# Kernel tuning notes

Measured on AMD Instinct MI355X. Metric: run time of the kernel, lower is better.

## Reference

```python
import jax, jax.numpy as jnp
import numpy as np

N = 100000
R = 32
E = 3200000
EMB = 128
H = 32
B = 16
C = 16

def setup_inputs() -> dict:
    key = jax.random.key(0)
    ks = jax.random.split(key, 10)
    def xavier(k, shape):
        fan_in, fan_out = shape[-2], shape[-1]
        gain = jnp.sqrt(2.0)  # relu gain
        std = gain * jnp.sqrt(2.0 / (fan_in + fan_out))
        return jax.random.normal(k, shape, jnp.float32) * std
    return {
        'embeddings': xavier(ks[0], (N, EMB)),
        'comps1': xavier(ks[1], (R, B)),
        'bases1': xavier(ks[2], (B, EMB, H)),
        'comps2': xavier(ks[3], (R, B)),
        'bases2': xavier(ks[4], (B, H, C)),
        'bias1': jnp.zeros((H,), jnp.float32),
        'bias2': jnp.zeros((C,), jnp.float32),
        'rel': jax.random.randint(ks[5], (E,), 0, R, jnp.int32),
        'fr': jax.random.randint(ks[6], (E,), 0, N, jnp.int32),
        'to': jax.random.randint(ks[7], (E,), 0, N, jnp.int32),
    }

def reference(embeddings, comps1, bases1, comps2, bases2, bias1, bias2, rel, fr, to):
    n, emb = embeddings.shape
    r = comps1.shape[0]
    h = bases1.shape[2]
    # edge normalization: vals = 1 / rowsum of vertical adjacency, row = rel*n + fr
    seg = rel * n + fr  # [E]
    deg = jax.ops.segment_sum(jnp.ones_like(fr, jnp.float32), seg, num_segments=r * n)
    vals = 1.0 / deg[seg]  # [E]
    # layer 1: basis-composed weights, per-relation transform, hor-graph spmm
    w1 = jnp.einsum('rb,beh->reh', comps1, bases1)          # [r,emb,h]
    xw = jnp.einsum('ne,reh->rnh', embeddings, w1)           # [r,n,h]
    # hor_graph @ xw.view(r*n,h): hidden1[fr] += vals * xw[rel, to]
    hidden1 = jax.ops.segment_sum(vals[:, None] * xw[rel, to], fr, num_segments=n)  # [n,h]
    hidden1 = jax.nn.relu(hidden1 + bias1)
    # layer 2: ver-graph spmm then relation-combining einsum
    w2 = jnp.einsum('rb,bhc->rhc', comps2, bases2)           # [r,h,c]
    hidden2 = jax.ops.segment_sum(vals[:, None] * hidden1[to], seg, num_segments=r * n)
    hidden2 = hidden2.reshape(r, n, h)
    out = jnp.einsum('rhc,rnh->nc', w2, hidden2)             # [n,c]
    return out + bias2
```

## Files before the change

### kernel.cpp

```cpp
#include <hip/hip_runtime.h>

#define N_NODES 100000
#define N_PAD   100096
#define E_EDGES 3200000
#define NB      392
#define BCAP    12288
#define EPB     2048

typedef float f32x4 __attribute__((ext_vector_type(4)));
typedef __bf16 bf16x8 __attribute__((ext_vector_type(8)));

__device__ __forceinline__ float b2f(unsigned int u) {
    union { unsigned int i; float f; } x; x.i = u << 16; return x.f;
}
__device__ __forceinline__ unsigned short f2b(float f) {
    union { float f; unsigned int i; } x; x.f = f;
    unsigned int u = x.i + 0x7FFFu + ((x.i >> 16) & 1u);
    return (unsigned short)(u >> 16);
}

__global__ __launch_bounds__(256) void kcur(int* __restrict__ gCursor) {
    int id = blockIdx.x * 256 + threadIdx.x;
    if (id < NB) gCursor[id] = id * BCAP;
}

__global__ __launch_bounds__(256) void kemb(const float* __restrict__ emb,
                                            unsigned short* __restrict__ embb) {
    int id = blockIdx.x * 256 + threadIdx.x;
    if (id >= N_PAD * 128 / 8) return;
    size_t base = (size_t)id * 8;
    ushort4 o0 = {0, 0, 0, 0}, o1 = {0, 0, 0, 0};
    if (base < (size_t)N_NODES * 128) {
        float4 v0 = *(const float4*)(emb + base);
        float4 v1 = *(const float4*)(emb + base + 4);
        o0.x = f2b(v0.x); o0.y = f2b(v0.y); o0.z = f2b(v0.z); o0.w = f2b(v0.w);
        o1.x = f2b(v1.x); o1.y = f2b(v1.y); o1.z = f2b(v1.z); o1.w = f2b(v1.w);
    }
    *(ushort4*)(embb + base) = o0;
    *(ushort4*)(embb + base + 4) = o1;
}

__global__ __launch_bounds__(256) void kw1(const float* __restrict__ comps1,
                                           const float* __restrict__ bases1,
                                           unsigned short* __restrict__ w1T) {
    int id = blockIdx.x * 256 + threadIdx.x;
    if (id >= 1024 * 128) return;
    int k = id & 127, j = id >> 7;
    int r = j >> 5, h = j & 31;
    float s = 0.f;
#pragma unroll
    for (int b = 0; b < 16; b++)
        s += comps1[r * 16 + b] * bases1[b * 4096 + k * 32 + h];
    w1T[(size_t)j * 128 + k] = f2b(s);
}

__global__ __launch_bounds__(256) void kw2(const float* __restrict__ comps2,
                                           const float* __restrict__ bases2,
                                           unsigned short* __restrict__ w2T) {
    int id = blockIdx.x * 256 + threadIdx.x;
    if (id >= 512 * 32) return;
    int h = id & 31, j = id >> 5;
    int r = j >> 4, c = j & 15;
    float s = 0.f;
#pragma unroll
    for (int b = 0; b < 16; b++)
        s += comps2[r * 16 + b] * bases2[b * 512 + h * 16 + c];
    w2T[(size_t)j * 32 + h] = f2b(s);
}

__global__ __launch_bounds__(256) void kbinA(const int* __restrict__ rel,
                                             const int* __restrict__ fr,
                                             const int* __restrict__ to,
                                             int* __restrict__ gCursor,
                                             unsigned int* __restrict__ stage) {
    __shared__ int cnt[NB];
    __shared__ int base[NB];
    int tid = threadIdx.x;
    int g0 = blockIdx.x * (EPB / 4);
    for (int i = tid; i < NB; i += 256) cnt[i] = 0;
    __syncthreads();
#pragma unroll
    for (int i = 0; i < EPB / 1024; i++) {
        int g = g0 + i * 256 + tid;
        if (g < E_EDGES / 4) {
            int4 f4 = ((const int4*)fr)[g];
            atomicAdd(&cnt[f4.x >> 8], 1);
            atomicAdd(&cnt[f4.y >> 8], 1);
            atomicAdd(&cnt[f4.z >> 8], 1);
            atomicAdd(&cnt[f4.w >> 8], 1);
        }
    }
    __syncthreads();
    for (int i = tid; i < NB; i += 256) {
        base[i] = atomicAdd(&gCursor[i], cnt[i]);
        cnt[i] = 0;
    }
    __syncthreads();
#pragma unroll
    for (int i = 0; i < EPB / 1024; i++) {
        int g = g0 + i * 256 + tid;
        if (g < E_EDGES / 4) {
            int4 f4 = ((const int4*)fr)[g];
            int4 r4 = ((const int4*)rel)[g];
            int4 t4 = ((const int4*)to)[g];
            int fa[4] = {f4.x, f4.y, f4.z, f4.w};
            int ra[4] = {r4.x, r4.y, r4.z, r4.w};
            int ta[4] = {t4.x, t4.y, t4.z, t4.w};
#pragma unroll
            for (int u = 0; u < 4; u++) {
                int b = fa[u] >> 8;
                int rank = atomicAdd(&cnt[b], 1);
                stage[base[b] + rank] =
                    ((unsigned int)(fa[u] & 255) << 22) | ((unsigned int)ra[u] << 17) | (unsigned int)ta[u];
            }
        }
    }
}

__global__ __launch_bounds__(512) void kscan(const int* __restrict__ gCursor,
                                             int* __restrict__ bucketBase) {
    __shared__ int a[512], b[512];
    int t = threadIdx.x;
    int v = (t < NB) ? (gCursor[t] - t * BCAP) : 0;
    a[t] = v;
    __syncthreads();
    int* src = a; int* dst = b;
    for (int ofs = 1; ofs < 512; ofs <<= 1) {
        int x = src[t];
        if (t >= ofs) x += src[t - ofs];
        __syncthreads();
        dst[t] = x;
        __syncthreads();
        int* tmp = src; src = dst; dst = tmp;
    }
    if (t < NB) bucketBase[t] = src[t] - v;
}

__global__ __launch_bounds__(256) void kscatter2(const unsigned int* __restrict__ stage,
                                                 const int* __restrict__ gCursor,
                                                 const int* __restrict__ bucketBase,
                                                 int* __restrict__ rowptr,
                                                 unsigned int* __restrict__ packed) {
    __shared__ int hist[256], hexcl[256], rk[256], sa[256], sb[256];
    __shared__ int hist2[256 * 32];
    int b = blockIdx.x, t = threadIdx.x;
    int nb = gCursor[b] - b * BCAP;
    int sbase = b * BCAP;
    int gbase = bucketBase[b];
    int nb4 = nb >> 2;
    hist[t] = 0; rk[t] = 0;
    for (int i = t; i < 256 * 32; i += 256) hist2[i] = 0;
    __syncthreads();
    for (int i4 = t; i4 < nb4; i4 += 256) {
        uint4 p4 = ((const uint4*)(stage + sbase))[i4];
        unsigned int pa[4] = {p4.x, p4.y, p4.z, p4.w};
#pragma unroll
        for (int u = 0; u < 4; u++) {
            atomicAdd(&hist[pa[u] >> 22], 1);
            atomicAdd(&hist2[((pa[u] >> 22) << 5) | ((pa[u] >> 17) & 31)], 1);
        }
    }
    for (int i = (nb4 << 2) + t; i < nb; i += 256) {
        unsigned int pk = stage[sbase + i];
        atomicAdd(&hist[pk >> 22], 1);
        atomicAdd(&hist2[((pk >> 22) << 5) | ((pk >> 17) & 31)], 1);
    }
    __syncthreads();
    int v = hist[t];
    sa[t] = v;
    __syncthreads();
    int* src = sa; int* dst = sb;
    for (int ofs = 1; ofs < 256; ofs <<= 1) {
        int x = src[t];
        if (t >= ofs) x += src[t - ofs];
        __syncthreads();
        dst[t] = x;
        __syncthreads();
        int* tmp = src; src = dst; dst = tmp;
    }
    int excl = src[t] - v;
    hexcl[t] = excl;
    rowptr[b * 256 + t] = gbase + excl;
    __syncthreads();
    for (int i4 = t; i4 < nb4; i4 += 256) {
        uint4 p4 = ((const uint4*)(stage + sbase))[i4];
        unsigned int pa[4] = {p4.x, p4.y, p4.z, p4.w};
#pragma unroll
        for (int u = 0; u < 4; u++) {
            int frlo = pa[u] >> 22;
            int rank = atomicAdd(&rk[frlo], 1);
            int dg = min(hist2[(frlo << 5) | ((pa[u] >> 17) & 31)], 1023);
            packed[gbase + hexcl[frlo] + rank] = ((unsigned int)dg << 22) | (pa[u] & 0x3FFFFFu);
        }
    }
    for (int i = (nb4 << 2) + t; i < nb; i += 256) {
        unsigned int pk = stage[sbase + i];
        int frlo = pk >> 22;
        int rank = atomicAdd(&rk[frlo], 1);
        int dg = min(hist2[(frlo << 5) | ((pk >> 17) & 31)], 1023);
        packed[gbase + hexcl[frlo] + rank] = ((unsigned int)dg << 22) | (pk & 0x3FFFFFu);
    }
}

__global__ __launch_bounds__(256) void gemm1(const unsigned short* __restrict__ embb,
                                             const unsigned short* __restrict__ w1T,
                                             unsigned short* __restrict__ xw) {
    __shared__ unsigned short ldsT[4 * 16 * 136];
    int id = blockIdx.x;
    int xcd = id & 7, w = id >> 3;
    int bn = w & 15, mgl = w >> 4;
    int mg = mgl * 8 + xcd;
    if (mg >= 98) return;
    int lane = threadIdx.x & 63, wave = threadIdx.x >> 6;
    int m_ = lane & 15, q = lane >> 4;
    unsigned short* tw = &ldsT[wave * 16 * 136];
    bf16x8 B[4][4];
    const unsigned short* Bbase = w1T + (size_t)(bn * 64 + m_) * 128 + q * 8;
#pragma unroll
    for (int j = 0; j < 4; j++)
#pragma unroll
        for (int k0 = 0; k0 < 4; k0++)
            B[j][k0] = *(const bf16x8*)(Bbase + j * 16 * 128 + k0 * 32);
    int mrow0 = mg * 1024 + wave * 16;
    const unsigned short* Abase = embb + (size_t)(mrow0 + m_) * 128 + q * 8;
    bf16x8 a0[4], a1[4];
    if (mrow0 < N_PAD) {
#pragma unroll
        for (int k0 = 0; k0 < 4; k0++)
            a0[k0] = *(const bf16x8*)(Abase + k0 * 32);
    }
#pragma unroll
    for (int t = 0; t < 16; t++) {
        int m0 = mrow0 + t * 64;
        if (m0 >= N_PAD) break;
        bf16x8* acur = (t & 1) ? a1 : a0;
        bf16x8* anext = (t & 1) ? a0 : a1;
        if (t < 15 && m0 + 64 < N_PAD) {
#pragma unroll
            for (int k0 = 0; k0 < 4; k0++)
                anext[k0] = *(const bf16x8*)(Abase + (size_t)(t + 1) * 64 * 128 + k0 * 32);
        }
        f32x4 acc[4] = {};
#pragma unroll
        for (int k0 = 0; k0 < 4; k0++)
#pragma unroll
            for (int j = 0; j < 4; j++)
                acc[j] = __builtin_amdgcn_mfma_f32_16x16x32_bf16(B[j][k0], acur[k0], acc[j], 0, 0, 0);
#pragma unroll
        for (int jj = 0; jj < 4; jj++) {
            ushort4 s;
            s.x = f2b(acc[jj][0]); s.y = f2b(acc[jj][1]);
            s.z = f2b(acc[jj][2]); s.w = f2b(acc[jj][3]);
            *(ushort4*)(tw + m_ * 136 + jj * 16 + q * 4) = s;
        }
        __asm__ volatile("s_waitcnt lgkmcnt(0)" ::: "memory");
#pragma unroll
        for (int ri = 0; ri < 2; ri++) {
            int row = (lane >> 3) + ri * 8;
            int c = lane & 7;
            uint4 v = *(const uint4*)(tw + row * 136 + c * 8);
            int grow = m0 + row;
            if (grow < N_NODES)
                *(uint4*)(xw + (size_t)grow * 1024 + bn * 64 + c * 8) = v;
        }
        __asm__ volatile("s_waitcnt lgkmcnt(0)" ::: "memory");
    }
}

__global__ __launch_bounds__(256) void edge1csr(const unsigned int* __restrict__ packed,
                                                const int* __restrict__ rowptr,
                                                const unsigned short* __restrict__ xw,
                                                const float* __restrict__ bias1,
                                                unsigned short* __restrict__ h1b) {
    __shared__ unsigned int ebuf[4 * 64];
    __shared__ float vbuf[4 * 64];
    int wave = threadIdx.x >> 6, lane = threadIdx.x & 63;
    int f = blockIdx.x * 4 + wave;
    if (f >= N_NODES) return;
    int s = rowptr[f], k = rowptr[f + 1] - s;
    int sub = lane & 7, p = lane >> 3;
    f32x4 acc = {0.f, 0.f, 0.f, 0.f};
    for (int base = 0; base < k; base += 64) {
        int e = base + lane;
        if (e < k) {
            unsigned int pk = packed[s + e];
            ebuf[wave * 64 + lane] = pk;
            vbuf[wave * 64 + lane] = 1.0f / (float)(pk >> 22);
        }
        int cnum = min(64, k - base);
        int nst = (cnum + 7) >> 3;
#pragma unroll 4
        for (int i = 0; i < nst; i++) {
            int ei = (i << 3) + p;
            if (ei < cnum) {
                unsigned int pk = ebuf[wave * 64 + ei];
                float v = vbuf[wave * 64 + ei];
                int t_ = pk & 0x1FFFF, r = (pk >> 17) & 31;
                ushort4 raw = *(const ushort4*)(xw + (size_t)t_ * 1024 + (r << 5) + (sub << 2));
                acc.x += v * b2f(raw.x); acc.y += v * b2f(raw.y);
                acc.z += v * b2f(raw.z); acc.w += v * b2f(raw.w);
            }
        }
    }
#pragma unroll
    for (int ofs = 8; ofs < 64; ofs <<= 1) {
        acc.x += __shfl_xor(acc.x, ofs, 64);
        acc.y += __shfl_xor(acc.y, ofs, 64);
        acc.z += __shfl_xor(acc.z, ofs, 64);
        acc.w += __shfl_xor(acc.w, ofs, 64);
    }
    if (p == 0) {
        int h = sub << 2;
        ushort4 o;
        o.x = f2b(fmaxf(acc.x + bias1[h + 0], 0.f));
        o.y = f2b(fmaxf(acc.y + bias1[h + 1], 0.f));
        o.z = f2b(fmaxf(acc.z + bias1[h + 2], 0.f));
        o.w = f2b(fmaxf(acc.w + bias1[h + 3], 0.f));
        *(ushort4*)(h1b + (size_t)f * 32 + h) = o;
    }
}

__global__ __launch_bounds__(256) void gemm2(const unsigned short* __restrict__ h1b,
                                             const unsigned short* __restrict__ w2T,
                                             unsigned short* __restrict__ z) {
    __shared__ unsigned short ldsT[4 * 16 * 136];
    int id = blockIdx.x;
    int xcd = id & 7, w = id >> 3;
    int bn = w & 7, mgl = w >> 3;
    int mg = mgl * 8 + xcd;
    if (mg >= 98) return;
    int lane = threadIdx.x & 63, wave = threadIdx.x >> 6;
    int m_ = lane & 15, q = lane >> 4;
    unsigned short* tw = &ldsT[wave * 16 * 136];
    bf16x8 B[4];
    const unsigned short* Bbase = w2T + (size_t)(bn * 64 + m_) * 32 + q * 8;
#pragma unroll
    for (int j = 0; j < 4; j++)
        B[j] = *(const bf16x8*)(Bbase + j * 16 * 32);
    int mrow0 = mg * 1024 + wave * 32;
    const unsigned short* Abase = h1b + (size_t)(mrow0 + m_) * 32 + q * 8;
    bf16x8 a0[2], a1[2];
    if (mrow0 < N_PAD) {
        a0[0] = *(const bf16x8*)(Abase);
        a0[1] = *(const bf16x8*)(Abase + 16 * 32);
    }
#pragma unroll
    for (int t = 0; t < 8; t++) {
        int m0 = mrow0 + t * 128;
        if (m0 >= N_PAD) break;
        bf16x8* acur = (t & 1) ? a1 : a0;
        bf16x8* anext = (t & 1) ? a0 : a1;
        if (t < 7 && m0 + 128 < N_PAD) {
            anext[0] = *(const bf16x8*)(Abase + (size_t)(t + 1) * 128 * 32);
            anext[1] = *(const bf16x8*)(Abase + (size_t)(t + 1) * 128 * 32 + 16 * 32);
        }
        f32x4 acc[2][4] = {};
#pragma unroll
        for (int i = 0; i < 2; i++)
#pragma unroll
            for (int j = 0; j < 4; j++)
                acc[i][j] = __builtin_amdgcn_mfma_f32_16x16x32_bf16(B[j], acur[i], acc[i][j], 0, 0, 0);
#pragma unroll
        for (int i = 0; i < 2; i++) {
#pragma unroll
            for (int jj = 0; jj < 4; jj++) {
                ushort4 s;
                s.x = f2b(acc[i][jj][0]); s.y = f2b(acc[i][jj][1]);
                s.z = f2b(acc[i][jj][2]); s.w = f2b(acc[i][jj][3]);
                *(ushort4*)(tw + m_ * 136 + jj * 16 + q * 4) = s;
            }
            __asm__ volatile("s_waitcnt lgkmcnt(0)" ::: "memory");
#pragma unroll
            for (int ri = 0; ri < 2; ri++) {
                int row = (lane >> 3) + ri * 8;
                int c = lane & 7;
                uint4 v = *(const uint4*)(tw + row * 136 + c * 8);
                int grow = m0 + i * 16 + row;
                if (grow < N_NODES)
                    *(uint4*)(z + (size_t)grow * 512 + bn * 64 + c * 8) = v;
            }
            __asm__ volatile("s_waitcnt lgkmcnt(0)" ::: "memory");
        }
    }
}

__global__ __launch_bounds__(256) void edge2csr(const unsigned int* __restrict__ packed,
                                                const int* __restrict__ rowptr,
                                                const unsigned short* __restrict__ z,
                                                const float* __restrict__ bias2,
                                                float* __restrict__ out) {
    __shared__ unsigned int ebuf[4 * 64];
    __shared__ float vbuf[4 * 64];
    int wave = threadIdx.x >> 6, lane = threadIdx.x & 63;
    int f = blockIdx.x * 4 + wave;
    if (f >= N_NODES) return;
    int s = rowptr[f], k = rowptr[f + 1] - s;
    int sub = lane & 3, p = lane >> 2;
    f32x4 acc = {0.f, 0.f, 0.f, 0.f};
    for (int base = 0; base < k; base += 64) {
        int e = base + lane;
        if (e < k) {
            unsigned int pk = packed[s + e];
            ebuf[wave * 64 + lane] = pk;
            vbuf[wave * 64 + lane] = 1.0f / (float)(pk >> 22);
        }
        int cnum = min(64, k - base);
        int nst = (cnum + 15) >> 4;
#pragma unroll 4
        for (int i = 0; i < nst; i++) {
            int ei = (i << 4) + p;
            if (ei < cnum) {
                unsigned int pk = ebuf[wave * 64 + ei];
                float v = vbuf[wave * 64 + ei];
                int t_ = pk & 0x1FFFF, r = (pk >> 17) & 31;
                ushort4 raw = *(const ushort4*)(z + (size_t)t_ * 512 + (r << 4) + (sub << 2));
                acc.x += v * b2f(raw.x); acc.y += v * b2f(raw.y);
                acc.z += v * b2f(raw.z); acc.w += v * b2f(raw.w);
            }
        }
    }
#pragma unroll
    for (int ofs = 4; ofs < 64; ofs <<= 1) {
        acc.x += __shfl_xor(acc.x, ofs, 64);
        acc.y += __shfl_xor(acc.y, ofs, 64);
        acc.z += __shfl_xor(acc.z, ofs, 64);
        acc.w += __shfl_xor(acc.w, ofs, 64);
    }
    if (p == 0) {
        int c = sub << 2;
        float4 o;
        o.x = acc.x + bias2[c + 0];
        o.y = acc.y + bias2[c + 1];
        o.z = acc.z + bias2[c + 2];
        o.w = acc.w + bias2[c + 3];
        *(float4*)(out + (size_t)f * 16 + c) = o;
    }
}

extern "C" void kernel_launch(void* const* d_in, const int* in_sizes, int n_in,
                              void* d_out, int out_size, void* d_ws, size_t ws_size,
                              hipStream_t stream) {
    (void)in_sizes; (void)n_in; (void)out_size; (void)ws_size;
    const float* emb    = (const float*)d_in[0];
    const float* comps1 = (const float*)d_in[1];
    const float* bases1 = (const float*)d_in[2];
    const float* comps2 = (const float*)d_in[3];
    const float* bases2 = (const float*)d_in[4];
    const float* bias1  = (const float*)d_in[5];
    const float* bias2  = (const float*)d_in[6];
    const int* rel = (const int*)d_in[7];
    const int* fr  = (const int*)d_in[8];
    const int* to  = (const int*)d_in[9];
    float* out = (float*)d_out;
    char* ws = (char*)d_ws;

    int* gCursor         = (int*)(ws);
    int* bucketBase      = (int*)(ws + 2048);
    int* rowptr          = (int*)(ws + 4096);
    unsigned int* packed = (unsigned int*)(ws + 406528);
    unsigned short* h1b  = (unsigned short*)(ws + 13206528);
    unsigned short* w1T  = (unsigned short*)(ws + 19612672);
    unsigned short* w2T  = (unsigned short*)(ws + 19874816);
    unsigned short* embb = (unsigned short*)(ws + 19907584);
    unsigned short* xw   = (unsigned short*)(ws + 45532160);
    unsigned short* z    = xw;
    unsigned int* stage  = (unsigned int*)xw;

    kcur<<<2, 256, 0, stream>>>(gCursor);
    kemb<<<6256, 256, 0, stream>>>(emb, embb);
    kw1<<<512, 256, 0, stream>>>(comps1, bases1, w1T);
    kw2<<<64, 256, 0, stream>>>(comps2, bases2, w2T);
    kbinA<<<(E_EDGES + EPB - 1) / EPB, 256, 0, stream>>>(rel, fr, to, gCursor, stage);
    kscan<<<1, 512, 0, stream>>>(gCursor, bucketBase);
    kscatter2<<<NB, 256, 0, stream>>>(stage, gCursor, bucketBase, rowptr, packed);
    gemm1<<<1664, 256, 0, stream>>>(embb, w1T, xw);
    edge1csr<<<25000, 256, 0, stream>>>(packed, rowptr, xw, bias1, h1b);
    gemm2<<<832, 256, 0, stream>>>(h1b, w2T, z);
    edge2csr<<<25000, 256, 0, stream>>>(packed, rowptr, z, bias2, out);
}
```

Before: 462.7 us.

## Replace CSR build with bucketed edge lists and LDS-atomic aggregation

Result: slower. 1.360 ms (+193.9%).

```diff
diff --git a/kernel.cpp b/kernel.cpp
--- a/kernel.cpp
+++ b/kernel.cpp
@@ -3,8 +3,8 @@
 #define N_NODES 100000
 #define N_PAD   100096
 #define E_EDGES 3200000
-#define NB      392
-#define BCAP    12288
+#define NB      784
+#define BCAP    4864
 #define EPB     2048
 
 typedef float f32x4 __attribute__((ext_vector_type(4)));
@@ -15,29 +15,12 @@
 }
 __device__ __forceinline__ unsigned short f2b(float f) {
     union { float f; unsigned int i; } x; x.f = f;
-    unsigned int u = x.i + 0x7FFFu + ((x.i >> 16) & 1u);
-    return (unsigned short)(u >> 16);
+    return (unsigned short)((x.i + 0x8000u) >> 16);
 }
 
 __global__ __launch_bounds__(256) void kcur(int* __restrict__ gCursor) {
     int id = blockIdx.x * 256 + threadIdx.x;
     if (id < NB) gCursor[id] = id * BCAP;
-}
-
-__global__ __launch_bounds__(256) void kemb(const float* __restrict__ emb,
-                                            unsigned short* __restrict__ embb) {
-    int id = blockIdx.x * 256 + threadIdx.x;
-    if (id >= N_PAD * 128 / 8) return;
-    size_t base = (size_t)id * 8;
-    ushort4 o0 = {0, 0, 0, 0}, o1 = {0, 0, 0, 0};
-    if (base < (size_t)N_NODES * 128) {
-        float4 v0 = *(const float4*)(emb + base);
-        float4 v1 = *(const float4*)(emb + base + 4);
-        o0.x = f2b(v0.x); o0.y = f2b(v0.y); o0.z = f2b(v0.z); o0.w = f2b(v0.w);
-        o1.x = f2b(v1.x); o1.y = f2b(v1.y); o1.z = f2b(v1.z); o1.w = f2b(v1.w);
-    }
-    *(ushort4*)(embb + base) = o0;
-    *(ushort4*)(embb + base + 4) = o1;
 }
 
 __global__ __launch_bounds__(256) void kw1(const float* __restrict__ comps1,
@@ -79,27 +62,12 @@
     int g0 = blockIdx.x * (EPB / 4);
     for (int i = tid; i < NB; i += 256) cnt[i] = 0;
     __syncthreads();
-#pragma unroll
-    for (int i = 0; i < EPB / 1024; i++) {
+    unsigned int wd[8]; int bk[8], rk[8]; bool vld[2];
+#pragma unroll
+    for (int i = 0; i < 2; i++) {
         int g = g0 + i * 256 + tid;
-        if (g < E_EDGES / 4) {
-            int4 f4 = ((const int4*)fr)[g];
-            atomicAdd(&cnt[f4.x >> 8], 1);
-            atomicAdd(&cnt[f4.y >> 8], 1);
-            atomicAdd(&cnt[f4.z >> 8], 1);
-            atomicAdd(&cnt[f4.w >> 8], 1);
-        }
-    }
-    __syncthreads();
-    for (int i = tid; i < NB; i += 256) {
-        base[i] = atomicAdd(&gCursor[i], cnt[i]);
-        cnt[i] = 0;
-    }
-    __syncthreads();
-#pragma unroll
-    for (int i = 0; i < EPB / 1024; i++) {
-        int g = g0 + i * 256 + tid;
-        if (g < E_EDGES / 4) {
+        vld[i] = (g < E_EDGES / 4);
+        if (vld[i]) {
             int4 f4 = ((const int4*)fr)[g];
             int4 r4 = ((const int4*)rel)[g];
             int4 t4 = ((const int4*)to)[g];
@@ -108,101 +76,31 @@
             int ta[4] = {t4.x, t4.y, t4.z, t4.w};
 #pragma unroll
             for (int u = 0; u < 4; u++) {
-                int b = fa[u] >> 8;
-                int rank = atomicAdd(&cnt[b], 1);
-                stage[base[b] + rank] =
-                    ((unsigned int)(fa[u] & 255) << 22) | ((unsigned int)ra[u] << 17) | (unsigned int)ta[u];
-            }
-        }
-    }
-}
-
-__global__ __launch_bounds__(512) void kscan(const int* __restrict__ gCursor,
-                                             int* __restrict__ bucketBase) {
-    __shared__ int a[512], b[512];
-    int t = threadIdx.x;
-    int v = (t < NB) ? (gCursor[t] - t * BCAP) : 0;
-    a[t] = v;
-    __syncthreads();
-    int* src = a; int* dst = b;
-    for (int ofs = 1; ofs < 512; ofs <<= 1) {
-        int x = src[t];
-        if (t >= ofs) x += src[t - ofs];
-        __syncthreads();
-        dst[t] = x;
-        __syncthreads();
-        int* tmp = src; src = dst; dst = tmp;
-    }
-    if (t < NB) bucketBase[t] = src[t] - v;
-}
-
-__global__ __launch_bounds__(256) void kscatter2(const unsigned int* __restrict__ stage,
-                                                 const int* __restrict__ gCursor,
-                                                 const int* __restrict__ bucketBase,
-                                                 int* __restrict__ rowptr,
-                                                 unsigned int* __restrict__ packed) {
-    __shared__ int hist[256], hexcl[256], rk[256], sa[256], sb[256];
-    __shared__ int hist2[256 * 32];
-    int b = blockIdx.x, t = threadIdx.x;
-    int nb = gCursor[b] - b * BCAP;
-    int sbase = b * BCAP;
-    int gbase = bucketBase[b];
-    int nb4 = nb >> 2;
-    hist[t] = 0; rk[t] = 0;
-    for (int i = t; i < 256 * 32; i += 256) hist2[i] = 0;
-    __syncthreads();
-    for (int i4 = t; i4 < nb4; i4 += 256) {
-        uint4 p4 = ((const uint4*)(stage + sbase))[i4];
-        unsigned int pa[4] = {p4.x, p4.y, p4.z, p4.w};
-#pragma unroll
-        for (int u = 0; u < 4; u++) {
-            atomicAdd(&hist[pa[u] >> 22], 1);
-            atomicAdd(&hist2[((pa[u] >> 22) << 5) | ((pa[u] >> 17) & 31)], 1);
-        }
-    }
-    for (int i = (nb4 << 2) + t; i < nb; i += 256) {
-        unsigned int pk = stage[sbase + i];
-        atomicAdd(&hist[pk >> 22], 1);
-        atomicAdd(&hist2[((pk >> 22) << 5) | ((pk >> 17) & 31)], 1);
-    }
-    __syncthreads();
-    int v = hist[t];
-    sa[t] = v;
-    __syncthreads();
-    int* src = sa; int* dst = sb;
-    for (int ofs = 1; ofs < 256; ofs <<= 1) {
-        int x = src[t];
-        if (t >= ofs) x += src[t - ofs];
-        __syncthreads();
-        dst[t] = x;
-        __syncthreads();
-        int* tmp = src; src = dst; dst = tmp;
-    }
-    int excl = src[t] - v;
-    hexcl[t] = excl;
-    rowptr[b * 256 + t] = gbase + excl;
-    __syncthreads();
-    for (int i4 = t; i4 < nb4; i4 += 256) {
-        uint4 p4 = ((const uint4*)(stage + sbase))[i4];
-        unsigned int pa[4] = {p4.x, p4.y, p4.z, p4.w};
-#pragma unroll
-        for (int u = 0; u < 4; u++) {
-            int frlo = pa[u] >> 22;
-            int rank = atomicAdd(&rk[frlo], 1);
-            int dg = min(hist2[(frlo << 5) | ((pa[u] >> 17) & 31)], 1023);
-            packed[gbase + hexcl[frlo] + rank] = ((unsigned int)dg << 22) | (pa[u] & 0x3FFFFFu);
-        }
-    }
-    for (int i = (nb4 << 2) + t; i < nb; i += 256) {
-        unsigned int pk = stage[sbase + i];
-        int frlo = pk >> 22;
-        int rank = atomicAdd(&rk[frlo], 1);
-        int dg = min(hist2[(frlo << 5) | ((pk >> 17) & 31)], 1023);
-        packed[gbase + hexcl[frlo] + rank] = ((unsigned int)dg << 22) | (pk & 0x3FFFFFu);
-    }
-}
-
-__global__ __launch_bounds__(256) void gemm1(const unsigned short* __restrict__ embb,
+                int ix = i * 4 + u;
+                bk[ix] = fa[u] >> 7;
+                wd[ix] = ((unsigned int)(fa[u] & 127) << 22) |
+                         ((unsigned int)ra[u] << 17) | (unsigned int)ta[u];
+                rk[ix] = atomicAdd(&cnt[bk[ix]], 1);
+            }
+        }
+    }
+    __syncthreads();
+    for (int i = tid; i < NB; i += 256)
+        base[i] = atomicAdd(&gCursor[i], cnt[i]);
+    __syncthreads();
+#pragma unroll
+    for (int i = 0; i < 2; i++) {
+        if (vld[i]) {
+#pragma unroll
+            for (int u = 0; u < 4; u++) {
+                int ix = i * 4 + u;
+                stage[base[bk[ix]] + rk[ix]] = wd[ix];
+            }
+        }
+    }
+}
+
+__global__ __launch_bounds__(256) void gemm1(const float* __restrict__ emb,
                                              const unsigned short* __restrict__ w1T,
                                              unsigned short* __restrict__ xw) {
     __shared__ unsigned short ldsT[4 * 16 * 136];
@@ -222,30 +120,49 @@
         for (int k0 = 0; k0 < 4; k0++)
             B[j][k0] = *(const bf16x8*)(Bbase + j * 16 * 128 + k0 * 32);
     int mrow0 = mg * 1024 + wave * 16;
-    const unsigned short* Abase = embb + (size_t)(mrow0 + m_) * 128 + q * 8;
-    bf16x8 a0[4], a1[4];
-    if (mrow0 < N_PAD) {
-#pragma unroll
-        for (int k0 = 0; k0 < 4; k0++)
-            a0[k0] = *(const bf16x8*)(Abase + k0 * 32);
+    float4 af[2][8];
+    {
+        int row = min(mrow0 + m_, N_NODES - 1);
+        const float* ap = emb + (size_t)row * 128 + q * 8;
+#pragma unroll
+        for (int k0 = 0; k0 < 4; k0++) {
+            af[0][k0 * 2]     = *(const float4*)(ap + k0 * 32);
+            af[0][k0 * 2 + 1] = *(const float4*)(ap + k0 * 32 + 4);
+        }
     }
 #pragma unroll
     for (int t = 0; t < 16; t++) {
         int m0 = mrow0 + t * 64;
         if (m0 >= N_PAD) break;
-        bf16x8* acur = (t & 1) ? a1 : a0;
-        bf16x8* anext = (t & 1) ? a0 : a1;
+        float4* cur = af[t & 1];
+        float4* nxt = af[(t + 1) & 1];
         if (t < 15 && m0 + 64 < N_PAD) {
-#pragma unroll
-            for (int k0 = 0; k0 < 4; k0++)
-                anext[k0] = *(const bf16x8*)(Abase + (size_t)(t + 1) * 64 * 128 + k0 * 32);
+            int row = min(mrow0 + (t + 1) * 64 + m_, N_NODES - 1);
+            const float* ap = emb + (size_t)row * 128 + q * 8;
+#pragma unroll
+            for (int k0 = 0; k0 < 4; k0++) {
+                nxt[k0 * 2]     = *(const float4*)(ap + k0 * 32);
+                nxt[k0 * 2 + 1] = *(const float4*)(ap + k0 * 32 + 4);
+            }
+        }
+        bf16x8 a[4];
+#pragma unroll
+        for (int k0 = 0; k0 < 4; k0++) {
+            ushort4 lo, hi;
+            lo.x = f2b(cur[k0 * 2].x); lo.y = f2b(cur[k0 * 2].y);
+            lo.z = f2b(cur[k0 * 2].z); lo.w = f2b(cur[k0 * 2].w);
+            hi.x = f2b(cur[k0 * 2 + 1].x); hi.y = f2b(cur[k0 * 2 + 1].y);
+            hi.z = f2b(cur[k0 * 2 + 1].z); hi.w = f2b(cur[k0 * 2 + 1].w);
+            union { ushort4 s[2]; bf16x8 v; } pk;
+            pk.s[0] = lo; pk.s[1] = hi;
+            a[k0] = pk.v;
         }
         f32x4 acc[4] = {};
 #pragma unroll
         for (int k0 = 0; k0 < 4; k0++)
 #pragma unroll
             for (int j = 0; j < 4; j++)
-                acc[j] = __builtin_amdgcn_mfma_f32_16x16x32_bf16(B[j][k0], acur[k0], acc[j], 0, 0, 0);
+                acc[j] = __builtin_amdgcn_mfma_f32_16x16x32_bf16(B[j][k0], a[k0], acc[j], 0, 0, 0);
 #pragma unroll
         for (int jj = 0; jj < 4; jj++) {
             ushort4 s;
@@ -267,56 +184,59 @@
     }
 }
 
-__global__ __launch_bounds__(256) void edge1csr(const unsigned int* __restrict__ packed,
-                                                const int* __restrict__ rowptr,
+__global__ __launch_bounds__(256) void edge1bkt(const unsigned int* __restrict__ stage,
+                                                const int* __restrict__ gCursor,
                                                 const unsigned short* __restrict__ xw,
                                                 const float* __restrict__ bias1,
                                                 unsigned short* __restrict__ h1b) {
-    __shared__ unsigned int ebuf[4 * 64];
-    __shared__ float vbuf[4 * 64];
-    int wave = threadIdx.x >> 6, lane = threadIdx.x & 63;
-    int f = blockIdx.x * 4 + wave;
-    if (f >= N_NODES) return;
-    int s = rowptr[f], k = rowptr[f + 1] - s;
+    __shared__ int hist2[128 * 33];
+    __shared__ float hacc[128 * 33];
+    int b = blockIdx.x, tid = threadIdx.x;
+    int nb = gCursor[b] - b * BCAP;
+    const unsigned int* sb = stage + (size_t)b * BCAP;
+    for (int i = tid; i < 128 * 33; i += 256) { hist2[i] = 0; hacc[i] = 0.f; }
+    __syncthreads();
+    int nb4 = nb >> 2;
+    for (int i4 = tid; i4 < nb4; i4 += 256) {
+        uint4 p4 = ((const uint4*)sb)[i4];
+        unsigned int pa[4] = {p4.x, p4.y, p4.z, p4.w};
+#pragma unroll
+        for (int u = 0; u < 4; u++)
+            atomicAdd(&hist2[(pa[u] >> 22) * 33 + ((pa[u] >> 17) & 31)], 1);
+    }
+    for (int i = (nb4 << 2) + tid; i < nb; i += 256) {
+        unsigned int pk = sb[i];
+        atomicAdd(&hist2[(pk >> 22) * 33 + ((pk >> 17) & 31)], 1);
+    }
+    __syncthreads();
+    int lane = tid & 63, wave = tid >> 6;
     int sub = lane & 7, p = lane >> 3;
-    f32x4 acc = {0.f, 0.f, 0.f, 0.f};
-    for (int base = 0; base < k; base += 64) {
-        int e = base + lane;
-        if (e < k) {
-            unsigned int pk = packed[s + e];
-            ebuf[wave * 64 + lane] = pk;
-            vbuf[wave * 64 + lane] = 1.0f / (float)(pk >> 22);
-        }
-        int cnum = min(64, k - base);
-        int nst = (cnum + 7) >> 3;
-#pragma unroll 4
-        for (int i = 0; i < nst; i++) {
-            int ei = (i << 3) + p;
-            if (ei < cnum) {
-                unsigned int pk = ebuf[wave * 64 + ei];
-                float v = vbuf[wave * 64 + ei];
-                int t_ = pk & 0x1FFFF, r = (pk >> 17) & 31;
-                ushort4 raw = *(const ushort4*)(xw + (size_t)t_ * 1024 + (r << 5) + (sub << 2));
-                acc.x += v * b2f(raw.x); acc.y += v * b2f(raw.y);
-                acc.z += v * b2f(raw.z); acc.w += v * b2f(raw.w);
-            }
-        }
-    }
-#pragma unroll
-    for (int ofs = 8; ofs < 64; ofs <<= 1) {
-        acc.x += __shfl_xor(acc.x, ofs, 64);
-        acc.y += __shfl_xor(acc.y, ofs, 64);
-        acc.z += __shfl_xor(acc.z, ofs, 64);
-        acc.w += __shfl_xor(acc.w, ofs, 64);
-    }
-    if (p == 0) {
-        int h = sub << 2;
-        ushort4 o;
-        o.x = f2b(fmaxf(acc.x + bias1[h + 0], 0.f));
-        o.y = f2b(fmaxf(acc.y + bias1[h + 1], 0.f));
-        o.z = f2b(fmaxf(acc.z + bias1[h + 2], 0.f));
-        o.w = f2b(fmaxf(acc.w + bias1[h + 3], 0.f));
-        *(ushort4*)(h1b + (size_t)f * 32 + h) = o;
+    for (int base = wave * 8; base < nb; base += 32) {
+        int e = base + p;
+        if (e < nb) {
+            unsigned int pk = sb[e];
+            int frlo = pk >> 22, r = (pk >> 17) & 31, t_ = pk & 0x1FFFF;
+            float v = 1.0f / (float)hist2[frlo * 33 + r];
+            ushort4 raw = *(const ushort4*)(xw + (size_t)t_ * 1024 + (r << 5) + (sub << 2));
+            float* hp = &hacc[frlo * 33 + 0];
+            atomicAdd(hp + (sub << 2) + 0, v * b2f(raw.x));
+            atomicAdd(hp + (sub << 2) + 1, v * b2f(raw.y));
+            atomicAdd(hp + (sub << 2) + 2, v * b2f(raw.z));
+            atomicAdd(hp + (sub << 2) + 3, v * b2f(raw.w));
+        }
+    }
+    __syncthreads();
+    for (int i = tid; i < 128 * 8; i += 256) {
+        int row = i >> 3, cq = (i & 7) << 2;
+        int f = b * 128 + row;
+        if (f < N_NODES) {
+            ushort4 o;
+            o.x = f2b(fmaxf(hacc[row * 33 + cq + 0] + bias1[cq + 0], 0.f));
+            o.y = f2b(fmaxf(hacc[row * 33 + cq + 1] + bias1[cq + 1], 0.f));
+            o.z = f2b(fmaxf(hacc[row * 33 + cq + 2] + bias1[cq + 2], 0.f));
+            o.w = f2b(fmaxf(hacc[row * 33 + cq + 3] + bias1[cq + 3], 0.f));
+            *(ushort4*)(h1b + (size_t)f * 32 + cq) = o;
+        }
     }
 }
 
@@ -384,56 +304,60 @@
     }
 }
 
-__global__ __launch_bounds__(256) void edge2csr(const unsigned int* __restrict__ packed,
-                                                const int* __restrict__ rowptr,
+__global__ __launch_bounds__(256) void edge2bkt(const unsigned int* __restrict__ stage,
+                                                const int* __restrict__ gCursor,
                                                 const unsigned short* __restrict__ z,
                                                 const float* __restrict__ bias2,
                                                 float* __restrict__ out) {
-    __shared__ unsigned int ebuf[4 * 64];
-    __shared__ float vbuf[4 * 64];
-    int wave = threadIdx.x >> 6, lane = threadIdx.x & 63;
-    int f = blockIdx.x * 4 + wave;
-    if (f >= N_NODES) return;
-    int s = rowptr[f], k = rowptr[f + 1] - s;
+    __shared__ int hist2[128 * 33];
+    __shared__ float oacc[128 * 17];
+    int b = blockIdx.x, tid = threadIdx.x;
+    int nb = gCursor[b] - b * BCAP;
+    const unsigned int* sb = stage + (size_t)b * BCAP;
+    for (int i = tid; i < 128 * 33; i += 256) hist2[i] = 0;
+    for (int i = tid; i < 128 * 17; i += 256) oacc[i] = 0.f;
+    __syncthreads();
+    int nb4 = nb >> 2;
+    for (int i4 = tid; i4 < nb4; i4 += 256) {
+        uint4 p4 = ((const uint4*)sb)[i4];
+        unsigned int pa[4] = {p4.x, p4.y, p4.z, p4.w};
+#pragma unroll
+        for (int u = 0; u < 4; u++)
+            atomicAdd(&hist2[(pa[u] >> 22) * 33 + ((pa[u] >> 17) & 31)], 1);
+    }
+    for (int i = (nb4 << 2) + tid; i < nb; i += 256) {
+        unsigned int pk = sb[i];
+        atomicAdd(&hist2[(pk >> 22) * 33 + ((pk >> 17) & 31)], 1);
+    }
+    __syncthreads();
+    int lane = tid & 63, wave = tid >> 6;
     int sub = lane & 3, p = lane >> 2;
-    f32x4 acc = {0.f, 0.f, 0.f, 0.f};
-    for (int base = 0; base < k; base += 64) {
-        int e = base + lane;
-        if (e < k) {
-            unsigned int pk = packed[s + e];
-            ebuf[wave * 64 + lane] = pk;
-            vbuf[wave * 64 + lane] = 1.0f / (float)(pk >> 22);
-        }
-        int cnum = min(64, k - base);
-        int nst = (cnum + 15) >> 4;
-#pragma unroll 4
-        for (int i = 0; i < nst; i++) {
-            int ei = (i << 4) + p;
-            if (ei < cnum) {
-                unsigned int pk = ebuf[wave * 64 + ei];
-                float v = vbuf[wave * 64 + ei];
-                int t_ = pk & 0x1FFFF, r = (pk >> 17) & 31;
-                ushort4 raw = *(const ushort4*)(z + (size_t)t_ * 512 + (r << 4) + (sub << 2));
-                acc.x += v * b2f(raw.x); acc.y += v * b2f(raw.y);
-                acc.z += v * b2f(raw.z); acc.w += v * b2f(raw.w);
-            }
-        }
-    }
-#pragma unroll
-    for (int ofs = 4; ofs < 64; ofs <<= 1) {
-        acc.x += __shfl_xor(acc.x, ofs, 64);
-        acc.y += __shfl_xor(acc.y, ofs, 64);
-        acc.z += __shfl_xor(acc.z, ofs, 64);
-        acc.w += __shfl_xor(acc.w, ofs, 64);
-    }
-    if (p == 0) {
-        int c = sub << 2;
-        float4 o;
-        o.x = acc.x + bias2[c + 0];
-        o.y = acc.y + bias2[c + 1];
-        o.z = acc.z + bias2[c + 2];
-        o.w = acc.w + bias2[c + 3];
-        *(float4*)(out + (size_t)f * 16 + c) = o;
+    for (int base = wave * 16; base < nb; base += 64) {
+        int e = base + p;
+        if (e < nb) {
+            unsigned int pk = sb[e];
+            int frlo = pk >> 22, r = (pk >> 17) & 31, t_ = pk & 0x1FFFF;
+            float v = 1.0f / (float)hist2[frlo * 33 + r];
+            ushort4 raw = *(const ushort4*)(z + (size_t)t_ * 512 + (r << 4) + (sub << 2));
+            float* op = &oacc[frlo * 17 + 0];
+            atomicAdd(op + (sub << 2) + 0, v * b2f(raw.x));
+            atomicAdd(op + (sub << 2) + 1, v * b2f(raw.y));
+            atomicAdd(op + (sub << 2) + 2, v * b2f(raw.z));
+            atomicAdd(op + (sub << 2) + 3, v * b2f(raw.w));
+        }
+    }
+    __syncthreads();
+    for (int i = tid; i < 128 * 4; i += 256) {
+        int row = i >> 2, cq = (i & 3) << 2;
+        int f = b * 128 + row;
+        if (f < N_NODES) {
+            float4 o;
+            o.x = oacc[row * 17 + cq + 0] + bias2[cq + 0];
+            o.y = oacc[row * 17 + cq + 1] + bias2[cq + 1];
+            o.z = oacc[row * 17 + cq + 2] + bias2[cq + 2];
+            o.w = oacc[row * 17 + cq + 3] + bias2[cq + 3];
+            *(float4*)(out + (size_t)f * 16 + cq) = o;
+        }
     }
 }
 
@@ -455,26 +379,19 @@
     char* ws = (char*)d_ws;
 
     int* gCursor         = (int*)(ws);
-    int* bucketBase      = (int*)(ws + 2048);
-    int* rowptr          = (int*)(ws + 4096);
-    unsigned int* packed = (unsigned int*)(ws + 406528);
-    unsigned short* h1b  = (unsigned short*)(ws + 13206528);
-    unsigned short* w1T  = (unsigned short*)(ws + 19612672);
-    unsigned short* w2T  = (unsigned short*)(ws + 19874816);
-    unsigned short* embb = (unsigned short*)(ws + 19907584);
-    unsigned short* xw   = (unsigned short*)(ws + 45532160);
+    unsigned short* h1b  = (unsigned short*)(ws + 4096);
+    unsigned short* w1T  = (unsigned short*)(ws + 6410240);
+    unsigned short* w2T  = (unsigned short*)(ws + 6672384);
+    unsigned int* stage  = (unsigned int*)(ws + 6705152);
+    unsigned short* xw   = (unsigned short*)(ws + 21959680);
     unsigned short* z    = xw;
-    unsigned int* stage  = (unsigned int*)xw;
-
-    kcur<<<2, 256, 0, stream>>>(gCursor);
-    kemb<<<6256, 256, 0, stream>>>(emb, embb);
+
+    kcur<<<4, 256, 0, stream>>>(gCursor);
     kw1<<<512, 256, 0, stream>>>(comps1, bases1, w1T);
     kw2<<<64, 256, 0, stream>>>(comps2, bases2, w2T);
     kbinA<<<(E_EDGES + EPB - 1) / EPB, 256, 0, stream>>>(rel, fr, to, gCursor, stage);
-    kscan<<<1, 512, 0, stream>>>(gCursor, bucketBase);
-    kscatter2<<<NB, 256, 0, stream>>>(stage, gCursor, bucketBase, rowptr, packed);
-    gemm1<<<1664, 256, 0, stream>>>(embb, w1T, xw);
-    edge1csr<<<25000, 256, 0, stream>>>(packed, rowptr, xw, bias1, h1b);
+    gemm1<<<1664, 256, 0, stream>>>(emb, w1T, xw);
+    edge1bkt<<<NB, 256, 0, stream>>>(stage, gCursor, xw, bias1, h1b);
     gemm2<<<832, 256, 0, stream>>>(h1b, w2T, z);
-    edge2csr<<<25000, 256, 0, stream>>>(packed, rowptr, z, bias2, out);
-}
+    edge2bkt<<<NB, 256, 0, stream>>>(stage, gCursor, z, bias2, out);
+}
```
